# Performance work log

Hardware: AMD Instinct MI355X
Metric: run time of the kernel (lower is better)

Reference implementation:

```python
import jax, jax.numpy as jnp
import numpy as np

NUM_HEADS = 32
NUM_KV_HEADS = 8
HEAD_DIM = 128
SCALE = 1.0 / float(np.sqrt(128.0))
LENS = [1024, 896, 768, 512]          # variable sequence lengths (batch=4)
MAX_SEQLEN = 1024
NUM_SLOTS = 16384                      # 64 blocks * block_size 256
NEG_INF = -1e30


def setup_inputs() -> dict:
    key = jax.random.key(0)
    k0, k1, k2 = jax.random.split(key, 3)
    total = int(sum(LENS))
    q = jax.random.normal(k0, (total, NUM_HEADS, HEAD_DIM), dtype=jnp.float32)
    k = jax.random.normal(k1, (total, NUM_KV_HEADS, HEAD_DIM), dtype=jnp.float32)
    v = jax.random.normal(k2, (total, NUM_KV_HEADS, HEAD_DIM), dtype=jnp.float32)
    k_cache = jnp.zeros((NUM_SLOTS, NUM_KV_HEADS, HEAD_DIM), dtype=jnp.float32)
    v_cache = jnp.zeros((NUM_SLOTS, NUM_KV_HEADS, HEAD_DIM), dtype=jnp.float32)
    slot_mapping = jnp.arange(total, dtype=jnp.int32)
    cu = jnp.concatenate([jnp.zeros((1,), jnp.int32),
                          jnp.cumsum(jnp.array(LENS, dtype=jnp.int32))])
    return {"q": q, "k": k, "v": v, "k_cache": k_cache, "v_cache": v_cache,
            "slot_mapping": slot_mapping, "cu_seqlens_q": cu, "cu_seqlens_k": cu,
            "max_seqlen": MAX_SEQLEN}


def _varlen_prefill_attention(q, k, v, cu_q, cu_k, max_seqlen):
    # q: [T, H, D]; k, v: [T, Hkv, D]; packed variable-length sequences.
    total = q.shape[0]
    B = cu_q.shape[0] - 1
    G = NUM_HEADS // NUM_KV_HEADS  # GQA group size
    lens_q = cu_q[1:] - cu_q[:-1]
    lens_k = cu_k[1:] - cu_k[:-1]
    pos = jnp.arange(max_seqlen)[None, :]                     # [1, S]
    q_idx = jnp.clip(cu_q[:-1, None] + pos, 0, total - 1)     # [B, S]
    k_idx = jnp.clip(cu_k[:-1, None] + pos, 0, total - 1)
    q_valid = pos < lens_q[:, None]                           # [B, S]
    k_valid = pos < lens_k[:, None]
    # Gather into padded [B, S, heads, D] and zero the padding.
    qp = jnp.where(q_valid[:, :, None, None], q[q_idx], 0)
    kp = jnp.where(k_valid[:, :, None, None], k[k_idx], 0)
    vp = jnp.where(k_valid[:, :, None, None], v[k_idx], 0)
    qp = qp.reshape(B, max_seqlen, NUM_KV_HEADS, G, HEAD_DIM)
    # logits: [B, Hkv, G, Sq, Sk]
    logits = jnp.einsum('bqhgd,bkhd->bhgqk', qp, kp) * SCALE
    causal = jnp.arange(max_seqlen)[:, None] >= jnp.arange(max_seqlen)[None, :]
    full_mask = causal[None, :, :] & q_valid[:, :, None] & k_valid[:, None, :]  # [B,Sq,Sk]
    logits = jnp.where(full_mask[:, None, None, :, :], logits, NEG_INF)
    probs = jax.nn.softmax(logits, axis=-1)
    outp = jnp.einsum('bhgqk,bkhd->bqhgd', probs, vp)
    outp = outp.reshape(B, max_seqlen, NUM_HEADS, HEAD_DIM)
    # Scatter padded output back to packed layout.
    dest = q_idx.reshape(-1)
    out_flat = jnp.where(q_valid.reshape(-1)[:, None, None],
                         outp.reshape(-1, NUM_HEADS, HEAD_DIM), 0)
    out = jnp.zeros((total, NUM_HEADS, HEAD_DIM), dtype=q.dtype)
    out = out.at[dest].add(out_flat)
    return out


def reference(q, k, v, k_cache, v_cache, slot_mapping, cu_seqlens_q, cu_seqlens_k, max_seqlen):
    # store_kv_to_cache (scatter into paged cache)
    valid = slot_mapping >= 0
    safe = jnp.where(valid, slot_mapping, 0)
    k_cache_new = k_cache.at[safe].set(k.astype(k_cache.dtype), mode='drop')
    v_cache_new = v_cache.at[safe].set(v.astype(v_cache.dtype), mode='drop')
    # prefill variable-length attention
    out = _varlen_prefill_attention(q, k, v, cu_seqlens_q, cu_seqlens_k, int(max_seqlen))
    return out, k_cache_new, v_cache_new
```

## Files before the change

kernel.cpp:

```cpp
#include <hip/hip_runtime.h>
#include <hip/hip_bf16.h>

#define NUM_HEADS 32
#define NUM_KV 8
#define GQA 4
#define HD 128
#define BM 64
#define BN 64
#define MAXS 1024

typedef unsigned short u16;
typedef unsigned int u32;
typedef __attribute__((ext_vector_type(8))) short bf16x8;
typedef __attribute__((ext_vector_type(4))) float f32x4;

__device__ __forceinline__ u16 f2bf(float f) {
    __hip_bfloat16 h = __float2bfloat16(f);
    return __builtin_bit_cast(u16, h);
}


__global__ void cache_copy(const float4* __restrict__ kci, const float4* __restrict__ vci,
                           float4* __restrict__ kco, float4* __restrict__ vco, int n4) {
    int i = blockIdx.x * blockDim.x + threadIdx.x;
    int stride = gridDim.x * blockDim.x;
    for (; i < n4; i += stride) {
        kco[i] = kci[i];
        vco[i] = vci[i];
    }
}

__global__ void kv_scatter(const float4* __restrict__ k, const float4* __restrict__ v,
                           const int* __restrict__ slots,
                           float4* __restrict__ kco, float4* __restrict__ vco, int nslots) {
    int t = blockIdx.x;
    int s = slots[t];
    if (s < 0 || s >= nslots) return;
    int i = threadIdx.x;
    kco[(size_t)s * 256 + i] = k[(size_t)t * 256 + i];
    vco[(size_t)s * 256 + i] = v[(size_t)t * 256 + i];
}


__global__ __launch_bounds__(512, 2) void attn_kernel(
    const float* __restrict__ q, const float* __restrict__ kk, const float* __restrict__ vv,
    const int* __restrict__ cu_q, const int* __restrict__ cu_k,
    float* __restrict__ out)
{
    __shared__ __align__(16) u16 Kt[BN * 136];
    __shared__ __align__(16) u16 Vt[HD * 72];
    __shared__ __align__(16) u16 Pb[8 * 16 * 72];

    const int qt = blockIdx.x, b = blockIdx.y, kvh = blockIdx.z;
    const int q0 = cu_q[b];
    const int Lq = cu_q[b + 1] - q0;
    const int k0 = cu_k[b];
    const int Lk = cu_k[b + 1] - k0;
    const int qbase = qt * BM;
    if (qbase >= Lq) return;

    const int tid = threadIdx.x;
    const int wave = tid >> 6;
    const int lane = tid & 63;
    const int c = lane & 15;
    const int quad = lane >> 4;
    const int h = kvh * GQA + (wave & 3);
    const int rhalf = wave >> 2;
    const int wrow0 = qbase + rhalf * 32;

    const float qs = 0.08838834764831845f * 1.44269504088896340f;
    bf16x8 qf[2][4];
#pragma unroll
    for (int rt = 0; rt < 2; ++rt) {
        int row = wrow0 + rt * 16 + c;
        int tok = q0 + (row < Lq ? row : Lq - 1);
        const float* qp = q + ((size_t)tok * NUM_HEADS + h) * HD + quad * 8;
#pragma unroll
        for (int kc = 0; kc < 4; ++kc) {
            float4 x = *(const float4*)(qp + kc * 32);
            float4 y = *(const float4*)(qp + kc * 32 + 4);
            union { bf16x8 v; u16 s[8]; } u;
            u.s[0] = f2bf(x.x * qs); u.s[1] = f2bf(x.y * qs);
            u.s[2] = f2bf(x.z * qs); u.s[3] = f2bf(x.w * qs);
            u.s[4] = f2bf(y.x * qs); u.s[5] = f2bf(y.y * qs);
            u.s[6] = f2bf(y.z * qs); u.s[7] = f2bf(y.w * qs);
            qf[rt][kc] = u.v;
        }
    }

    f32x4 Oacc[2][8];
    f32x4 m_i[2], l_i[2];
#pragma unroll
    for (int rt = 0; rt < 2; ++rt) {
        m_i[rt] = (f32x4)(-3.0e38f);
        l_i[rt] = (f32x4)(0.0f);
#pragma unroll
        for (int nt = 0; nt < 8; ++nt) Oacc[rt][nt] = (f32x4)(0.0f);
    }

    const int kmax = min(qbase + BM, Lk);
    const int ntile = (kmax + BN - 1) / BN;
    const int stkey = tid >> 3;
    const int stg = tid & 7;

    for (int it = 0; it < ntile; ++it) {
        const int kbase = it * BN;
        __syncthreads();
        {
            int kp = kbase + stkey;
            int tok = k0 + (kp < Lk ? kp : Lk - 1);
            const float* kg = kk + ((size_t)tok * NUM_KV + kvh) * HD + stg * 16;
            float4 a = ((const float4*)kg)[0];
            float4 b4 = ((const float4*)kg)[1];
            float4 c4 = ((const float4*)kg)[2];
            float4 d4 = ((const float4*)kg)[3];
            u32 p0 = f2bf(a.x)  | ((u32)f2bf(a.y)  << 16);
            u32 p1 = f2bf(a.z)  | ((u32)f2bf(a.w)  << 16);
            u32 p2 = f2bf(b4.x) | ((u32)f2bf(b4.y) << 16);
            u32 p3 = f2bf(b4.z) | ((u32)f2bf(b4.w) << 16);
            u32 p4 = f2bf(c4.x) | ((u32)f2bf(c4.y) << 16);
            u32 p5 = f2bf(c4.z) | ((u32)f2bf(c4.w) << 16);
            u32 p6 = f2bf(d4.x) | ((u32)f2bf(d4.y) << 16);
            u32 p7 = f2bf(d4.z) | ((u32)f2bf(d4.w) << 16);
            int g0 = (2 * stg)     ^ (stkey & 7);
            int g1 = (2 * stg + 1) ^ (stkey & 7);
            *(uint4*)&Kt[stkey * 136 + g0 * 8] = make_uint4(p0, p1, p2, p3);
            *(uint4*)&Kt[stkey * 136 + g1 * 8] = make_uint4(p4, p5, p6, p7);
        }
        {
            int vp = kbase + lane;
            int tok = k0 + (vp < Lk ? vp : Lk - 1);
            const float* vg = vv + ((size_t)tok * NUM_KV + kvh) * HD + wave * 16;
            int kb = lane >> 3, ko = lane & 7;
#pragma unroll
            for (int i = 0; i < 4; ++i) {
                float4 x = ((const float4*)vg)[i];
                int dim = wave * 16 + i * 4;
                Vt[(dim + 0) * 72 + ((kb ^ ((dim + 0) & 7)) * 8) + ko] = f2bf(x.x);
                Vt[(dim + 1) * 72 + ((kb ^ ((dim + 1) & 7)) * 8) + ko] = f2bf(x.y);
                Vt[(dim + 2) * 72 + ((kb ^ ((dim + 2) & 7)) * 8) + ko] = f2bf(x.z);
                Vt[(dim + 3) * 72 + ((kb ^ ((dim + 3) & 7)) * 8) + ko] = f2bf(x.w);
            }
        }
        __syncthreads();

        f32x4 S[2][4];
#pragma unroll
        for (int rt = 0; rt < 2; ++rt)
#pragma unroll
            for (int nt = 0; nt < 4; ++nt) S[rt][nt] = (f32x4)(0.0f);
#pragma unroll
        for (int nt = 0; nt < 4; ++nt) {
            int key = nt * 16 + c;
#pragma unroll
            for (int kc = 0; kc < 4; ++kc) {
                bf16x8 kf = *(const bf16x8*)&Kt[key * 136 + (((kc * 4 + quad) ^ (c & 7)) * 8)];
                S[0][nt] = __builtin_amdgcn_mfma_f32_16x16x32_bf16(qf[0][kc], kf, S[0][nt], 0, 0, 0);
                S[1][nt] = __builtin_amdgcn_mfma_f32_16x16x32_bf16(qf[1][kc], kf, S[1][nt], 0, 0, 0);
            }
        }

        bf16x8 pf[2][2];
#pragma unroll
        for (int rt = 0; rt < 2; ++rt) {
            int rtb = wrow0 + rt * 16;
            bool notfull = !((kbase + BN <= rtb + 1) && (kbase + BN <= Lk));
            if (notfull) {
                int qp4 = rtb + quad * 4;
#pragma unroll
                for (int nt = 0; nt < 4; ++nt) {
                    int kp = kbase + nt * 16 + c;
                    bool kval = kp < Lk;
#pragma unroll
                    for (int r = 0; r < 4; ++r)
                        if (!(kval && kp <= qp4 + r)) S[rt][nt][r] = -3.0e38f;
                }
            }
            f32x4 rm;
#pragma unroll
            for (int r = 0; r < 4; ++r)
                rm[r] = fmaxf(fmaxf(S[rt][0][r], S[rt][1][r]), fmaxf(S[rt][2][r], S[rt][3][r]));
#pragma unroll
            for (int d2 = 1; d2 < 16; d2 <<= 1)
#pragma unroll
                for (int r = 0; r < 4; ++r)
                    rm[r] = fmaxf(rm[r], __shfl_xor(rm[r], d2));
            f32x4 mn, al;
#pragma unroll
            for (int r = 0; r < 4; ++r) {
                mn[r] = fmaxf(m_i[rt][r], rm[r]);
                al[r] = exp2f(m_i[rt][r] - mn[r]);
            }
            m_i[rt] = mn;
            f32x4 rs = (f32x4)(0.0f);
#pragma unroll
            for (int nt = 0; nt < 4; ++nt)
#pragma unroll
                for (int r = 0; r < 4; ++r) {
                    float p = exp2f(S[rt][nt][r] - mn[r]);
                    S[rt][nt][r] = p;
                    rs[r] += p;
                }
#pragma unroll
            for (int d2 = 1; d2 < 16; d2 <<= 1)
#pragma unroll
                for (int r = 0; r < 4; ++r)
                    rs[r] += __shfl_xor(rs[r], d2);
#pragma unroll
            for (int r = 0; r < 4; ++r)
                l_i[rt][r] = l_i[rt][r] * al[r] + rs[r];
#pragma unroll
            for (int nt = 0; nt < 8; ++nt)
#pragma unroll
                for (int r = 0; r < 4; ++r)
                    Oacc[rt][nt][r] *= al[r];
            u16* pb = &Pb[wave * (16 * 72)];
#pragma unroll
            for (int nt = 0; nt < 4; ++nt)
#pragma unroll
                for (int r = 0; r < 4; ++r)
                    pb[(quad * 4 + r) * 72 + nt * 16 + c] = f2bf(S[rt][nt][r]);
            asm volatile("s_waitcnt lgkmcnt(0)" ::: "memory");
            pf[rt][0] = *(const bf16x8*)&pb[c * 72 + quad * 8];
            pf[rt][1] = *(const bf16x8*)&pb[c * 72 + 32 + quad * 8];
            asm volatile("" ::: "memory");
        }

#pragma unroll
        for (int nt = 0; nt < 8; ++nt) {
            int dim = nt * 16 + c;
#pragma unroll
            for (int kc = 0; kc < 2; ++kc) {
                bf16x8 vf = *(const bf16x8*)&Vt[dim * 72 + (((kc * 4 + quad) ^ (c & 7)) * 8)];
                Oacc[0][nt] = __builtin_amdgcn_mfma_f32_16x16x32_bf16(pf[0][kc], vf, Oacc[0][nt], 0, 0, 0);
                Oacc[1][nt] = __builtin_amdgcn_mfma_f32_16x16x32_bf16(pf[1][kc], vf, Oacc[1][nt], 0, 0, 0);
            }
        }
    }

#pragma unroll
    for (int rt = 0; rt < 2; ++rt) {
        f32x4 li;
#pragma unroll
        for (int r = 0; r < 4; ++r) li[r] = 1.0f / l_i[rt][r];
#pragma unroll
        for (int r = 0; r < 4; ++r) {
            int row = wrow0 + rt * 16 + quad * 4 + r;
            if (row < Lq) {
                float* op = out + ((size_t)(q0 + row) * NUM_HEADS + h) * HD + c;
#pragma unroll
                for (int nt = 0; nt < 8; ++nt)
                    op[nt * 16] = Oacc[rt][nt][r] * li[r];
            }
        }
    }
}

extern "C" void kernel_launch(void* const* d_in, const int* in_sizes, int n_in,
                              void* d_out, int out_size, void* d_ws, size_t ws_size,
                              hipStream_t stream) {
    const float* q   = (const float*)d_in[0];
    const float* k   = (const float*)d_in[1];
    const float* v   = (const float*)d_in[2];
    const float* kci = (const float*)d_in[3];
    const float* vci = (const float*)d_in[4];
    const int* slot  = (const int*)d_in[5];
    const int* cuq   = (const int*)d_in[6];
    const int* cuk   = (const int*)d_in[7];

    int total  = in_sizes[0] / (NUM_HEADS * HD);
    int nslots = in_sizes[3] / (NUM_KV * HD);
    int nseq   = in_sizes[6] - 1;

    float* out = (float*)d_out;
    float* kco = out + (size_t)total * NUM_HEADS * HD;
    float* vco = kco + (size_t)nslots * NUM_KV * HD;

    int n4 = nslots * NUM_KV * HD / 4;
    cache_copy<<<4096, 256, 0, stream>>>((const float4*)kci, (const float4*)vci,
                                         (float4*)kco, (float4*)vco, n4);
    kv_scatter<<<total, 256, 0, stream>>>((const float4*)k, (const float4*)v, slot,
                                          (float4*)kco, (float4*)vco, nslots);
    attn_kernel<<<dim3(MAXS / BM, nseq, NUM_KV), 512, 0, stream>>>(q, k, v, cuq, cuk, out);
}
```

Baseline: 492.3 us.

## Fuse cache update into attention kernel via inverse slot map and halve query tile

New measurement: 399.3 us. 1.23x faster.

```diff
diff --git a/kernel.cpp b/kernel.cpp
--- a/kernel.cpp
+++ b/kernel.cpp
@@ -5,14 +5,19 @@
 #define NUM_KV 8
 #define GQA 4
 #define HD 128
-#define BM 64
+#define BM 32
 #define BN 64
 #define MAXS 1024
+#define QTMAX (MAXS / BM)
+#define KSTR 136
+#define VSTR 72
+#define PSTR 72
 
 typedef unsigned short u16;
 typedef unsigned int u32;
 typedef __attribute__((ext_vector_type(8))) short bf16x8;
 typedef __attribute__((ext_vector_type(4))) float f32x4;
+typedef __attribute__((ext_vector_type(4))) float f4v;
 
 __device__ __forceinline__ u16 f2bf(float f) {
     __hip_bfloat16 h = __float2bfloat16(f);
@@ -20,38 +25,77 @@
 }
 
 
-__global__ void cache_copy(const float4* __restrict__ kci, const float4* __restrict__ vci,
-                           float4* __restrict__ kco, float4* __restrict__ vco, int n4) {
+__global__ void inv_init(int* __restrict__ inv, int n) {
     int i = blockIdx.x * blockDim.x + threadIdx.x;
-    int stride = gridDim.x * blockDim.x;
-    for (; i < n4; i += stride) {
-        kco[i] = kci[i];
-        vco[i] = vci[i];
-    }
-}
-
-__global__ void kv_scatter(const float4* __restrict__ k, const float4* __restrict__ v,
-                           const int* __restrict__ slots,
-                           float4* __restrict__ kco, float4* __restrict__ vco, int nslots) {
-    int t = blockIdx.x;
-    int s = slots[t];
-    if (s < 0 || s >= nslots) return;
-    int i = threadIdx.x;
-    kco[(size_t)s * 256 + i] = k[(size_t)t * 256 + i];
-    vco[(size_t)s * 256 + i] = v[(size_t)t * 256 + i];
-}
-
-
-__global__ __launch_bounds__(512, 2) void attn_kernel(
+    for (; i < n; i += gridDim.x * blockDim.x) inv[i] = -1;
+}
+
+__global__ void inv_scatter(const int* __restrict__ slot, int* __restrict__ inv,
+                            int total, int nslots) {
+    int i = blockIdx.x * blockDim.x + threadIdx.x;
+    if (i < total) {
+        int s = slot[i];
+        if (s >= 0 && s < nslots) inv[s] = i;
+    }
+}
+
+
+__global__ __launch_bounds__(256, 2) void fused_kernel(
     const float* __restrict__ q, const float* __restrict__ kk, const float* __restrict__ vv,
+    const float* __restrict__ kci, const float* __restrict__ vci,
+    const int* __restrict__ inv,
     const int* __restrict__ cu_q, const int* __restrict__ cu_k,
-    float* __restrict__ out)
+    float* __restrict__ out, float* __restrict__ kco, float* __restrict__ vco,
+    int nseq, int nslots, int W, int nattn)
 {
-    __shared__ __align__(16) u16 Kt[BN * 136];
-    __shared__ __align__(16) u16 Vt[HD * 72];
-    __shared__ __align__(16) u16 Pb[8 * 16 * 72];
-
-    const int qt = blockIdx.x, b = blockIdx.y, kvh = blockIdx.z;
+    __shared__ __align__(16) u16 Kt[BN * KSTR];
+    __shared__ __align__(16) u16 Vt[HD * VSTR];
+    __shared__ __align__(16) u16 Pb[4 * 32 * PSTR];
+
+    const int bid = blockIdx.x;
+    const int tid = threadIdx.x;
+
+    int u, wid = -1;
+    if (bid < 3 * W) {
+        int t3 = bid / 3, r3 = bid - 3 * t3;
+        if (r3 == 2) { wid = t3; u = -1; }
+        else u = t3 * 2 + r3;
+    } else {
+        u = 2 * W + (bid - 3 * W);
+    }
+
+    if (wid >= 0) {
+        const f4v* k4   = (const f4v*)kk;
+        const f4v* v4   = (const f4v*)vv;
+        const f4v* kci4 = (const f4v*)kci;
+        const f4v* vci4 = (const f4v*)vci;
+        f4v* kco4 = (f4v*)kco;
+        f4v* vco4 = (f4v*)vco;
+        for (int s = wid; s < nslots; s += W) {
+            int t = inv[s];
+            size_t so = (size_t)s * 256 + tid;
+            f4v kv, vvv;
+            if (t >= 0) {
+                size_t to = (size_t)t * 256 + tid;
+                kv  = k4[to];
+                vvv = v4[to];
+            } else {
+                kv  = __builtin_nontemporal_load(&kci4[so]);
+                vvv = __builtin_nontemporal_load(&vci4[so]);
+            }
+            __builtin_nontemporal_store(kv,  &kco4[so]);
+            __builtin_nontemporal_store(vvv, &vco4[so]);
+        }
+        return;
+    }
+
+    if (u >= nattn) return;
+    const int per = nseq * NUM_KV;
+    const int qt = QTMAX - 1 - u / per;
+    const int inner = u % per;
+    const int kvh = inner % NUM_KV;
+    const int b = inner / NUM_KV;
+
     const int q0 = cu_q[b];
     const int Lq = cu_q[b + 1] - q0;
     const int k0 = cu_k[b];
@@ -59,32 +103,29 @@
     const int qbase = qt * BM;
     if (qbase >= Lq) return;
 
-    const int tid = threadIdx.x;
     const int wave = tid >> 6;
     const int lane = tid & 63;
     const int c = lane & 15;
     const int quad = lane >> 4;
-    const int h = kvh * GQA + (wave & 3);
-    const int rhalf = wave >> 2;
-    const int wrow0 = qbase + rhalf * 32;
+    const int h = kvh * GQA + wave;
 
     const float qs = 0.08838834764831845f * 1.44269504088896340f;
     bf16x8 qf[2][4];
 #pragma unroll
     for (int rt = 0; rt < 2; ++rt) {
-        int row = wrow0 + rt * 16 + c;
+        int row = qbase + rt * 16 + c;
         int tok = q0 + (row < Lq ? row : Lq - 1);
         const float* qp = q + ((size_t)tok * NUM_HEADS + h) * HD + quad * 8;
 #pragma unroll
         for (int kc = 0; kc < 4; ++kc) {
             float4 x = *(const float4*)(qp + kc * 32);
             float4 y = *(const float4*)(qp + kc * 32 + 4);
-            union { bf16x8 v; u16 s[8]; } u;
-            u.s[0] = f2bf(x.x * qs); u.s[1] = f2bf(x.y * qs);
-            u.s[2] = f2bf(x.z * qs); u.s[3] = f2bf(x.w * qs);
-            u.s[4] = f2bf(y.x * qs); u.s[5] = f2bf(y.y * qs);
-            u.s[6] = f2bf(y.z * qs); u.s[7] = f2bf(y.w * qs);
-            qf[rt][kc] = u.v;
+            union { bf16x8 v; u16 s[8]; } uu;
+            uu.s[0] = f2bf(x.x * qs); uu.s[1] = f2bf(x.y * qs);
+            uu.s[2] = f2bf(x.z * qs); uu.s[3] = f2bf(x.w * qs);
+            uu.s[4] = f2bf(y.x * qs); uu.s[5] = f2bf(y.y * qs);
+            uu.s[6] = f2bf(y.z * qs); uu.s[7] = f2bf(y.w * qs);
+            qf[rt][kc] = uu.v;
         }
     }
 
@@ -100,46 +141,50 @@
 
     const int kmax = min(qbase + BM, Lk);
     const int ntile = (kmax + BN - 1) / BN;
-    const int stkey = tid >> 3;
-    const int stg = tid & 7;
+
+    const int kst_key = tid >> 2;
+    const int kst_g   = tid & 3;
+    const int vp2     = tid >> 3;
+    const int vdg     = tid & 7;
+    const int vgran   = vp2 >> 2;
+    const int vko     = (vp2 & 3) * 2;
 
     for (int it = 0; it < ntile; ++it) {
         const int kbase = it * BN;
         __syncthreads();
         {
-            int kp = kbase + stkey;
+            int kp = kbase + kst_key;
             int tok = k0 + (kp < Lk ? kp : Lk - 1);
-            const float* kg = kk + ((size_t)tok * NUM_KV + kvh) * HD + stg * 16;
-            float4 a = ((const float4*)kg)[0];
-            float4 b4 = ((const float4*)kg)[1];
-            float4 c4 = ((const float4*)kg)[2];
-            float4 d4 = ((const float4*)kg)[3];
-            u32 p0 = f2bf(a.x)  | ((u32)f2bf(a.y)  << 16);
-            u32 p1 = f2bf(a.z)  | ((u32)f2bf(a.w)  << 16);
-            u32 p2 = f2bf(b4.x) | ((u32)f2bf(b4.y) << 16);
-            u32 p3 = f2bf(b4.z) | ((u32)f2bf(b4.w) << 16);
-            u32 p4 = f2bf(c4.x) | ((u32)f2bf(c4.y) << 16);
-            u32 p5 = f2bf(c4.z) | ((u32)f2bf(c4.w) << 16);
-            u32 p6 = f2bf(d4.x) | ((u32)f2bf(d4.y) << 16);
-            u32 p7 = f2bf(d4.z) | ((u32)f2bf(d4.w) << 16);
-            int g0 = (2 * stg)     ^ (stkey & 7);
-            int g1 = (2 * stg + 1) ^ (stkey & 7);
-            *(uint4*)&Kt[stkey * 136 + g0 * 8] = make_uint4(p0, p1, p2, p3);
-            *(uint4*)&Kt[stkey * 136 + g1 * 8] = make_uint4(p4, p5, p6, p7);
+            const float* kg = kk + ((size_t)tok * NUM_KV + kvh) * HD + kst_g * 32;
+            u16* krow = &Kt[kst_key * KSTR];
+#pragma unroll
+            for (int j = 0; j < 4; ++j) {
+                float4 x = ((const float4*)kg)[2 * j];
+                float4 y = ((const float4*)kg)[2 * j + 1];
+                uint4 p;
+                p.x = f2bf(x.x) | ((u32)f2bf(x.y) << 16);
+                p.y = f2bf(x.z) | ((u32)f2bf(x.w) << 16);
+                p.z = f2bf(y.x) | ((u32)f2bf(y.y) << 16);
+                p.w = f2bf(y.z) | ((u32)f2bf(y.w) << 16);
+                *(uint4*)&krow[(kst_g * 4 + j) * 8] = p;
+            }
         }
         {
-            int vp = kbase + lane;
-            int tok = k0 + (vp < Lk ? vp : Lk - 1);
-            const float* vg = vv + ((size_t)tok * NUM_KV + kvh) * HD + wave * 16;
-            int kb = lane >> 3, ko = lane & 7;
-#pragma unroll
-            for (int i = 0; i < 4; ++i) {
-                float4 x = ((const float4*)vg)[i];
-                int dim = wave * 16 + i * 4;
-                Vt[(dim + 0) * 72 + ((kb ^ ((dim + 0) & 7)) * 8) + ko] = f2bf(x.x);
-                Vt[(dim + 1) * 72 + ((kb ^ ((dim + 1) & 7)) * 8) + ko] = f2bf(x.y);
-                Vt[(dim + 2) * 72 + ((kb ^ ((dim + 2) & 7)) * 8) + ko] = f2bf(x.z);
-                Vt[(dim + 3) * 72 + ((kb ^ ((dim + 3) & 7)) * 8) + ko] = f2bf(x.w);
+            int key0 = kbase + 2 * vp2;
+            int tok0 = k0 + (key0     < Lk ? key0     : Lk - 1);
+            int tok1 = k0 + (key0 + 1 < Lk ? key0 + 1 : Lk - 1);
+            const float* va = vv + ((size_t)tok0 * NUM_KV + kvh) * HD + vdg * 16;
+            const float* vb = vv + ((size_t)tok1 * NUM_KV + kvh) * HD + vdg * 16;
+            int pos = ((vgran + vdg) & 7) * 8 + vko;
+#pragma unroll
+            for (int i4 = 0; i4 < 4; ++i4) {
+                float4 a = ((const float4*)va)[i4];
+                float4 bb = ((const float4*)vb)[i4];
+                int d0 = vdg * 16 + i4 * 4;
+                *(u32*)&Vt[(d0 + 0) * VSTR + pos] = f2bf(a.x) | ((u32)f2bf(bb.x) << 16);
+                *(u32*)&Vt[(d0 + 1) * VSTR + pos] = f2bf(a.y) | ((u32)f2bf(bb.y) << 16);
+                *(u32*)&Vt[(d0 + 2) * VSTR + pos] = f2bf(a.z) | ((u32)f2bf(bb.z) << 16);
+                *(u32*)&Vt[(d0 + 3) * VSTR + pos] = f2bf(a.w) | ((u32)f2bf(bb.w) << 16);
             }
         }
         __syncthreads();
@@ -154,16 +199,16 @@
             int key = nt * 16 + c;
 #pragma unroll
             for (int kc = 0; kc < 4; ++kc) {
-                bf16x8 kf = *(const bf16x8*)&Kt[key * 136 + (((kc * 4 + quad) ^ (c & 7)) * 8)];
+                bf16x8 kf = *(const bf16x8*)&Kt[key * KSTR + (kc * 4 + quad) * 8];
                 S[0][nt] = __builtin_amdgcn_mfma_f32_16x16x32_bf16(qf[0][kc], kf, S[0][nt], 0, 0, 0);
                 S[1][nt] = __builtin_amdgcn_mfma_f32_16x16x32_bf16(qf[1][kc], kf, S[1][nt], 0, 0, 0);
             }
         }
 
-        bf16x8 pf[2][2];
+        u16* pb = &Pb[wave * (32 * PSTR)];
 #pragma unroll
         for (int rt = 0; rt < 2; ++rt) {
-            int rtb = wrow0 + rt * 16;
+            int rtb = qbase + rt * 16;
             bool notfull = !((kbase + BN <= rtb + 1) && (kbase + BN <= Lk));
             if (notfull) {
                 int qp4 = rtb + quad * 4;
@@ -214,24 +259,27 @@
 #pragma unroll
                 for (int r = 0; r < 4; ++r)
                     Oacc[rt][nt][r] *= al[r];
-            u16* pb = &Pb[wave * (16 * 72)];
 #pragma unroll
             for (int nt = 0; nt < 4; ++nt)
 #pragma unroll
                 for (int r = 0; r < 4; ++r)
-                    pb[(quad * 4 + r) * 72 + nt * 16 + c] = f2bf(S[rt][nt][r]);
-            asm volatile("s_waitcnt lgkmcnt(0)" ::: "memory");
-            pf[rt][0] = *(const bf16x8*)&pb[c * 72 + quad * 8];
-            pf[rt][1] = *(const bf16x8*)&pb[c * 72 + 32 + quad * 8];
-            asm volatile("" ::: "memory");
-        }
+                    pb[(rt * 16 + quad * 4 + r) * PSTR + nt * 16 + c] = f2bf(S[rt][nt][r]);
+        }
+        asm volatile("s_waitcnt lgkmcnt(0)" ::: "memory");
+        bf16x8 pf[2][2];
+#pragma unroll
+        for (int rt = 0; rt < 2; ++rt) {
+            pf[rt][0] = *(const bf16x8*)&pb[(rt * 16 + c) * PSTR + quad * 8];
+            pf[rt][1] = *(const bf16x8*)&pb[(rt * 16 + c) * PSTR + 32 + quad * 8];
+        }
+        asm volatile("" ::: "memory");
 
 #pragma unroll
         for (int nt = 0; nt < 8; ++nt) {
             int dim = nt * 16 + c;
 #pragma unroll
             for (int kc = 0; kc < 2; ++kc) {
-                bf16x8 vf = *(const bf16x8*)&Vt[dim * 72 + (((kc * 4 + quad) ^ (c & 7)) * 8)];
+                bf16x8 vf = *(const bf16x8*)&Vt[dim * VSTR + (((kc * 4 + quad) + nt) & 7) * 8];
                 Oacc[0][nt] = __builtin_amdgcn_mfma_f32_16x16x32_bf16(pf[0][kc], vf, Oacc[0][nt], 0, 0, 0);
                 Oacc[1][nt] = __builtin_amdgcn_mfma_f32_16x16x32_bf16(pf[1][kc], vf, Oacc[1][nt], 0, 0, 0);
             }
@@ -245,7 +293,7 @@
         for (int r = 0; r < 4; ++r) li[r] = 1.0f / l_i[rt][r];
 #pragma unroll
         for (int r = 0; r < 4; ++r) {
-            int row = wrow0 + rt * 16 + quad * 4 + r;
+            int row = qbase + rt * 16 + quad * 4 + r;
             if (row < Lq) {
                 float* op = out + ((size_t)(q0 + row) * NUM_HEADS + h) * HD + c;
 #pragma unroll
@@ -276,10 +324,13 @@
     float* kco = out + (size_t)total * NUM_HEADS * HD;
     float* vco = kco + (size_t)nslots * NUM_KV * HD;
 
-    int n4 = nslots * NUM_KV * HD / 4;
-    cache_copy<<<4096, 256, 0, stream>>>((const float4*)kci, (const float4*)vci,
-                                         (float4*)kco, (float4*)vco, n4);
-    kv_scatter<<<total, 256, 0, stream>>>((const float4*)k, (const float4*)v, slot,
-                                          (float4*)kco, (float4*)vco, nslots);
-    attn_kernel<<<dim3(MAXS / BM, nseq, NUM_KV), 512, 0, stream>>>(q, k, v, cuq, cuk, out);
-}
+    int* inv = (int*)d_ws;
+    int nattn = QTMAX * nseq * NUM_KV;
+    int W = nattn / 2;
+    if (W > 512) W = 512;
+
+    inv_init<<<64, 256, 0, stream>>>(inv, nslots);
+    inv_scatter<<<(total + 255) / 256, 256, 0, stream>>>(slot, inv, total, nslots);
+    fused_kernel<<<nattn + W, 256, 0, stream>>>(q, k, v, kci, vci, inv, cuq, cuk,
+                                                out, kco, vco, nseq, nslots, W, nattn);
+}
```
